# Performance work log

Measured on AMD Instinct MI355X. Metric: run time of the kernel, lower is better.

Reference implementation:

```python
import jax, jax.numpy as jnp
import numpy as np

NU, NI = 100000, 100000   # num users / items
DU, DI = 128, 128         # input feature dims
H, O = 256, 256           # hidden_channels, out_channels
ER, EA = 500000, 500000   # edges: reviews, also_bought


def setup_inputs() -> dict:
    key = jax.random.key(0)
    ks = jax.random.split(key, 30)

    def W(k, i, o):
        return jax.random.normal(k, (i, o), jnp.float32) * np.float32(1.0 / np.sqrt(i))

    return {
        "x_user": jax.random.normal(ks[0], (NU, DU), jnp.float32),
        "x_item": jax.random.normal(ks[1], (NI, DI), jnp.float32),
        "src_rev": jax.random.randint(ks[2], (ER,), 0, NU, jnp.int32),
        "dst_rev": jax.random.randint(ks[3], (ER,), 0, NI, jnp.int32),
        "src_ab": jax.random.randint(ks[4], (EA,), 0, NI, jnp.int32),
        "dst_ab": jax.random.randint(ks[5], (EA,), 0, NI, jnp.int32),
        # layer 1 (SAGEConv per edge type): lin_l (neighbor), lin_r (root), bias on lin_l
        "Wl1_rev": W(ks[6], DU, H), "Wr1_rev": W(ks[7], DI, H), "b1_rev": jnp.zeros((H,), jnp.float32),
        "Wl1_rrev": W(ks[8], DI, H), "Wr1_rrev": W(ks[9], DU, H), "b1_rrev": jnp.zeros((H,), jnp.float32),
        "Wl1_ab": W(ks[10], DI, H), "Wr1_ab": W(ks[11], DI, H), "b1_ab": jnp.zeros((H,), jnp.float32),
        # layer 2
        "Wl2_rev": W(ks[12], H, O), "Wr2_rev": W(ks[13], H, O), "b2_rev": jnp.zeros((O,), jnp.float32),
        "Wl2_rrev": W(ks[14], H, O), "Wr2_rrev": W(ks[15], H, O), "b2_rrev": jnp.zeros((O,), jnp.float32),
        "Wl2_ab": W(ks[16], H, O), "Wr2_ab": W(ks[17], H, O), "b2_ab": jnp.zeros((O,), jnp.float32),
    }


def sage_conv(x_src, x_dst, src, dst, Wl, b, Wr):
    """PyG SAGEConv: lin_l(mean of neighbor feats) + lin_r(x_dst); mean of empty set = 0."""
    n_dst = x_dst.shape[0]
    msg_sum = jax.ops.segment_sum(x_src[src], dst, num_segments=n_dst)   # [n_dst, d_src]
    cnt = jax.ops.segment_sum(jnp.ones(dst.shape, x_src.dtype), dst, num_segments=n_dst)
    mean = msg_sum / jnp.maximum(cnt, 1.0)[:, None]
    return mean @ Wl + b + x_dst @ Wr


def reference(x_user, x_item, src_rev, dst_rev, src_ab, dst_ab,
              Wl1_rev, Wr1_rev, b1_rev, Wl1_rrev, Wr1_rrev, b1_rrev, Wl1_ab, Wr1_ab, b1_ab,
              Wl2_rev, Wr2_rev, b2_rev, Wl2_rrev, Wr2_rrev, b2_rrev, Wl2_ab, Wr2_ab, b2_ab):
    # layer 1 + HeteroConv sum aggregation across edge types per dst node type
    h_item = (sage_conv(x_user, x_item, src_rev, dst_rev, Wl1_rev, b1_rev, Wr1_rev)
              + sage_conv(x_item, x_item, src_ab, dst_ab, Wl1_ab, b1_ab, Wr1_ab))
    # rev_reviews = transpose of reviews: item -> user
    h_user = sage_conv(x_item, x_user, dst_rev, src_rev, Wl1_rrev, b1_rrev, Wr1_rrev)
    h_item = jax.nn.relu(h_item)
    h_user = jax.nn.relu(h_user)
    # layer 2
    o_item = (sage_conv(h_user, h_item, src_rev, dst_rev, Wl2_rev, b2_rev, Wr2_rev)
              + sage_conv(h_item, h_item, src_ab, dst_ab, Wl2_ab, b2_ab, Wr2_ab))
    o_user = sage_conv(h_item, h_user, dst_rev, src_rev, Wl2_rrev, b2_rrev, Wr2_rrev)
    return (o_user, o_item)
```

## Files before the change

kernel.cpp:

```cpp
#include <hip/hip_runtime.h>
#include <hip/hip_bf16.h>

#define NN    100000
#define MPAD  100096
#define ER_   500000
#define EA_   500000
#define NCH   25
#define F_RELU 2

typedef __attribute__((ext_vector_type(8))) _Float16 f16x8;
typedef __attribute__((ext_vector_type(4))) float f32x4;
typedef __attribute__((address_space(3))) uint lds_uint;
typedef const __attribute__((address_space(1))) uint g_uint;

union H8 { uint4 u; _Float16 h[8]; };
union H1 { _Float16 h; ushort u; };

__device__ __forceinline__ ushort f2h(float f) { H1 c; c.h = (_Float16)f; return c.u; }

__global__ void count3(const int* __restrict__ dst_rev, const int* __restrict__ dst_ab,
                       const int* __restrict__ src_rev, int* __restrict__ cnt ) {
    int i = blockIdx.x * blockDim.x + threadIdx.x;
    if (i < ER_)                 atomicAdd(&cnt[dst_rev[i]], 1);
    else if (i < ER_ + EA_)      atomicAdd(&cnt[NN + dst_ab[i - ER_]], 1);
    else if (i < ER_ + EA_ + ER_) atomicAdd(&cnt[2 * NN + src_rev[i - ER_ - EA_]], 1);
}

__global__ void fill3(const int* __restrict__ dst_rev, const int* __restrict__ src_rev,
                      const int* __restrict__ dst_ab, const int* __restrict__ src_ab,
                      const int* __restrict__ pA, const int* __restrict__ pB,
                      const int* __restrict__ pC, int* __restrict__ cur ,
                      int* __restrict__ colA, int* __restrict__ colB, int* __restrict__ colC) {
    int i = blockIdx.x * blockDim.x + threadIdx.x;
    if (i < ER_) {
        int d = dst_rev[i];
        colA[pA[d] + atomicAdd(&cur[d], 1)] = src_rev[i];
    } else if (i < ER_ + EA_) {
        int e = i - ER_, d = dst_ab[e];
        colB[pB[d] + atomicAdd(&cur[NN + d], 1)] = src_ab[e];
    } else if (i < ER_ + EA_ + ER_) {
        int e = i - ER_ - EA_, d = src_rev[e];
        colC[pC[d] + atomicAdd(&cur[2 * NN + d], 1)] = dst_rev[e];
    }
}

__global__ void scan_part(const int* __restrict__ cnt , int* __restrict__ part) {
    int b = blockIdx.x, a = b / NCH, c = b % NCH;
    const int* src = cnt + a * NN;
    int base = c * 4096 + threadIdx.x * 16;
    int s = 0;
    #pragma unroll
    for (int k = 0; k < 16; k += 4) {
        int i = base + k;
        if (i + 3 < NN) { int4 v = *(const int4*)(src + i); s += v.x + v.y + v.z + v.w; }
        else { for (int j = 0; j < 4; j++) if (i + j < NN) s += src[i + j]; }
    }
    __shared__ int ws[4];
    int lane = threadIdx.x & 63, wid = threadIdx.x >> 6;
    #pragma unroll
    for (int o = 32; o > 0; o >>= 1) s += __shfl_down(s, o, 64);
    if (lane == 0) ws[wid] = s;
    __syncthreads();
    if (threadIdx.x == 0) part[b] = ws[0] + ws[1] + ws[2] + ws[3];
}

__global__ void scan_off(const int* __restrict__ part, int* __restrict__ choff,
                         int* __restrict__ pA, int* __restrict__ pB, int* __restrict__ pC) {
    int a = threadIdx.x;
    if (a < 3) {
        int acc = 0;
        for (int c = 0; c < NCH; c++) { choff[a * NCH + c] = acc; acc += part[a * NCH + c]; }
        int* p = (a == 0) ? pA : (a == 1) ? pB : pC;
        p[NN] = acc;
    }
}

__global__ void scan_apply(const int* __restrict__ cnt, const int* __restrict__ choff,
                           int* __restrict__ pA, int* __restrict__ pB, int* __restrict__ pC) {
    int b = blockIdx.x, a = b / NCH, c = b % NCH;
    const int* src = cnt + a * NN;
    int* ptr = (a == 0) ? pA : (a == 1) ? pB : pC;
    int tid = threadIdx.x, lane = tid & 63, wid = tid >> 6;
    int base = c * 4096 + tid * 16;
    int v[16], s = 0;
    #pragma unroll
    for (int k = 0; k < 16; k++) { int i = base + k; v[k] = (i < NN) ? src[i] : 0; s += v[k]; }
    int isc = s;
    #pragma unroll
    for (int o = 1; o < 64; o <<= 1) { int t = __shfl_up(isc, o, 64); if (lane >= o) isc += t; }
    __shared__ int wsum[4];
    if (lane == 63) wsum[wid] = isc;
    __syncthreads();
    int woff = 0;
    for (int wj = 0; wj < wid; wj++) woff += wsum[wj];
    int excl = choff[a * NCH + c] + woff + (isc - s);
    #pragma unroll
    for (int k = 0; k < 16; k++) { int i = base + k; if (i < NN) ptr[i] = excl; excl += v[k]; }
}

struct PrepArgs {
    const float* xsrc[2]; ushort* xdst[2];
    const float* W0[10]; const float* W1[10]; ushort* T[10];
};

__global__ void prep_all(PrepArgs A) {
    const long CVB = (long)MPAD * 128 / 8 / 256;
    long b = blockIdx.x;
    if (b < 2 * CVB) {
        int which = (b >= CVB);
        long lb = b - which * CVB;
        long i = (lb * 256 + threadIdx.x) * 8;
        const float* x = A.xsrc[which];
        ushort* o = A.xdst[which];
        float4 v0 = {0.f,0.f,0.f,0.f}, v1 = {0.f,0.f,0.f,0.f};
        if (i < (long)NN * 128) { v0 = *(const float4*)(x + i); v1 = *(const float4*)(x + i + 4); }
        H8 r;
        r.h[0]=(_Float16)v0.x; r.h[1]=(_Float16)v0.y; r.h[2]=(_Float16)v0.z; r.h[3]=(_Float16)v0.w;
        r.h[4]=(_Float16)v1.x; r.h[5]=(_Float16)v1.y; r.h[6]=(_Float16)v1.z; r.h[7]=(_Float16)v1.w;
        *(uint4*)(o + i) = r.u;
        return;
    }
    long j = (b - 2 * CVB) * 256 + threadIdx.x;
    int idx, rem, K;
    if (j < 5 * 32768) { idx = j >> 15; rem = j & 32767; K = 128; }
    else {
        long j2 = j - 5 * 32768;
        if (j2 >= 5L * 65536) return;
        idx = 5 + (int)(j2 >> 16); rem = (int)(j2 & 65535); K = 256;
    }
    int k = rem >> 8, n = rem & 255;
    float v = A.W0[idx][rem];
    if (A.W1[idx]) v += A.W1[idx][rem];
    A.T[idx][n * K + k] = f2h(v);
}

__global__ void agg3_128(const ushort* __restrict__ xu, const ushort* __restrict__ xi,
                         const int* __restrict__ pA, const int* __restrict__ cA,
                         const int* __restrict__ pB, const int* __restrict__ cB,
                         const int* __restrict__ pC, const int* __restrict__ cC,
                         ushort* __restrict__ sA, ushort* __restrict__ sB,
                         ushort* __restrict__ sC) {
    const int SEG = MPAD * 16 / 256;
    int seg = blockIdx.x / SEG, lb = blockIdx.x % SEG;
    const ushort* x; const int* ptr; const int* col; ushort* out;
    if (seg == 0)      { x = xu; ptr = pA; col = cA; out = sA; }
    else if (seg == 1) { x = xi; ptr = pB; col = cB; out = sB; }
    else               { x = xi; ptr = pC; col = cC; out = sC; }
    int g = lb * 256 + threadIdx.x;
    int node = g >> 4, l = g & 15;
    if (node >= MPAD) return;
    size_t ob = (size_t)node * 128 + l * 8;
    if (node >= NN) { *(uint4*)(out + ob) = make_uint4(0,0,0,0); return; }
    int p0 = ptr[node], p1 = ptr[node + 1];
    float a[8] = {0.f,0.f,0.f,0.f,0.f,0.f,0.f,0.f};
    for (int e = p0; e < p1; ++e) {
        H8 v; v.u = *(const uint4*)(x + (size_t)col[e] * 128 + l * 8);
        #pragma unroll
        for (int k = 0; k < 8; k++) a[k] += (float)v.h[k];
    }
    float inv = (p1 > p0) ? 1.0f / (float)(p1 - p0) : 0.0f;
    H8 r;
    #pragma unroll
    for (int k = 0; k < 8; k++) r.h[k] = (_Float16)(a[k] * inv);
    *(uint4*)(out + ob) = r.u;
}

__global__ void agg3_256(const ushort* __restrict__ hU, const ushort* __restrict__ hI,
                         const int* __restrict__ pA, const int* __restrict__ cA,
                         const int* __restrict__ pB, const int* __restrict__ cB,
                         const int* __restrict__ pC, const int* __restrict__ cC,
                         ushort* __restrict__ sA, ushort* __restrict__ sB,
                         ushort* __restrict__ sC) {
    const int SEG = MPAD * 32 / 256;
    int seg = blockIdx.x / SEG, lb = blockIdx.x % SEG;
    const ushort* x; const int* ptr; const int* col; ushort* out;
    if (seg == 0)      { x = hU; ptr = pA; col = cA; out = sA; }
    else if (seg == 1) { x = hI; ptr = pB; col = cB; out = sB; }
    else               { x = hI; ptr = pC; col = cC; out = sC; }
    int g = lb * 256 + threadIdx.x;
    int node = g >> 5, l = g & 31;
    if (node >= MPAD) return;
    size_t ob = (size_t)node * 256 + l * 8;
    if (node >= NN) { *(uint4*)(out + ob) = make_uint4(0,0,0,0); return; }
    int p0 = ptr[node], p1 = ptr[node + 1];
    float a[8] = {0.f,0.f,0.f,0.f,0.f,0.f,0.f,0.f};
    for (int e = p0; e < p1; ++e) {
        H8 v; v.u = *(const uint4*)(x + (size_t)col[e] * 256 + l * 8);
        #pragma unroll
        for (int k = 0; k < 8; k++) a[k] += (float)v.h[k];
    }
    float inv = (p1 > p0) ? 1.0f / (float)(p1 - p0) : 0.0f;
    H8 r;
    #pragma unroll
    for (int k = 0; k < 8; k++) r.h[k] = (_Float16)(a[k] * inv);
    *(uint4*)(out + ob) = r.u;
}

struct GP {
    const ushort *A0, *W0, *A1, *W1, *A2, *W2;
    int ksh0, ksh1, ksh2;
    int c1, c2, S;
};

__global__ __launch_bounds__(256)
void gemm2x(GP Pa, const float* b0a, const float* b1a, float* Cfa, ushort* Cha, int fla,
            GP Pb, const float* b0b, const float* b1b, float* Cfb, ushort* Chb, int flb) {
    GP P; const float *b0, *b1; float* Cf; ushort* Ch; int flags;
    if (blockIdx.z == 0) { P = Pa; b0 = b0a; b1 = b1a; Cf = Cfa; Ch = Cha; flags = fla; }
    else                 { P = Pb; b0 = b0b; b1 = b1b; Cf = Cfb; Ch = Chb; flags = flb; }

    __shared__ ushort sA[128 * 64];
    __shared__ ushort sW[128 * 64];
    const int tid = threadIdx.x;
    const int m0 = blockIdx.x * 128, n0 = blockIdx.y * 128;
    const int lane = tid & 63, w = tid >> 6;
    const int wr = (w >> 1) * 64, wc = (w & 1) * 64;
    const int fcol = lane & 15, fq = lane >> 4;
    const int srow = tid >> 3, sc = tid & 7;

    f32x4 acc[4][4];
    #pragma unroll
    for (int i = 0; i < 4; i++)
        #pragma unroll
        for (int j = 0; j < 4; j++) acc[i][j] = (f32x4){0.f,0.f,0.f,0.f};

    #pragma unroll 1
    for (int t = 0; t < P.S; ++t) {
        int p = (t >= P.c1) + (t >= P.c2);
        const ushort* A = (p == 2) ? P.A2 : (p == 1) ? P.A1 : P.A0;
        const ushort* W = (p == 2) ? P.W2 : (p == 1) ? P.W1 : P.W0;
        int ksh  = (p == 2) ? P.ksh2 : (p == 1) ? P.ksh1 : P.ksh0;
        int base = (p == 2) ? P.c2 : (p == 1) ? P.c1 : 0;
        int k0 = (t - base) << 6;

        #pragma unroll
        for (int ii = 0; ii < 4; ++ii) {
            int row = ii * 32 + srow;
            int q = sc ^ (row & 7);
            const ushort* srcA = A + (((size_t)(m0 + row)) << ksh) + k0 + q * 8;
            const ushort* srcW = W + (((size_t)(n0 + row)) << ksh) + k0 + q * 8;
            __builtin_amdgcn_global_load_lds((g_uint*)srcA,
                (lds_uint*)(sA + row * 64 + sc * 8), 16, 0, 0);
            __builtin_amdgcn_global_load_lds((g_uint*)srcW,
                (lds_uint*)(sW + row * 64 + sc * 8), 16, 0, 0);
        }
        __syncthreads();

        #pragma unroll
        for (int kk = 0; kk < 2; ++kk) {
            f16x8 a[4], b[4];
            #pragma unroll
            for (int i = 0; i < 4; ++i) {
                int ra = wr + i * 16 + fcol;
                int s = (fq + kk * 4) ^ (ra & 7);
                a[i] = *(const f16x8*)(sA + ra * 64 + s * 8);
            }
            #pragma unroll
            for (int j = 0; j < 4; ++j) {
                int rw = wc + j * 16 + fcol;
                int s = (fq + kk * 4) ^ (rw & 7);
                b[j] = *(const f16x8*)(sW + rw * 64 + s * 8);
            }
            #pragma unroll
            for (int i = 0; i < 4; ++i)
                #pragma unroll
                for (int j = 0; j < 4; ++j)
                    acc[i][j] = __builtin_amdgcn_mfma_f32_16x16x32_f16(a[i], b[j], acc[i][j], 0, 0, 0);
        }
        __syncthreads();
    }

    const bool relu = flags & F_RELU;
    float bb[4];
    #pragma unroll
    for (int j = 0; j < 4; ++j) {
        int cg = n0 + wc + j * 16 + fcol;
        float v = 0.f;
        if (b0) v += b0[cg];
        if (b1) v += b1[cg];
        bb[j] = v;
    }
    #pragma unroll
    for (int i = 0; i < 4; ++i) {
        #pragma unroll
        for (int r = 0; r < 4; ++r) {
            int gm = m0 + wr + i * 16 + fq * 4 + r;
            if (gm >= NN) continue;
            size_t rowb = (size_t)gm * 256;
            #pragma unroll
            for (int j = 0; j < 4; ++j) {
                size_t idx = rowb + n0 + wc + j * 16 + fcol;
                float v = acc[i][j][r] + bb[j];
                if (relu) v = fmaxf(v, 0.f);
                if (Ch) Ch[idx] = f2h(v);
                else    Cf[idx] = v;
            }
        }
    }
}

extern "C" void kernel_launch(void* const* d_in, const int* in_sizes, int n_in,
                              void* d_out, int out_size, void* d_ws, size_t ws_size,
                              hipStream_t stream) {
    const float* x_user = (const float*)d_in[0];
    const float* x_item = (const float*)d_in[1];
    const int* src_rev  = (const int*)d_in[2];
    const int* dst_rev  = (const int*)d_in[3];
    const int* src_ab   = (const int*)d_in[4];
    const int* dst_ab   = (const int*)d_in[5];
    const float* Wl1_rev  = (const float*)d_in[6];
    const float* Wr1_rev  = (const float*)d_in[7];
    const float* b1_rev   = (const float*)d_in[8];
    const float* Wl1_rrev = (const float*)d_in[9];
    const float* Wr1_rrev = (const float*)d_in[10];
    const float* b1_rrev  = (const float*)d_in[11];
    const float* Wl1_ab   = (const float*)d_in[12];
    const float* Wr1_ab   = (const float*)d_in[13];
    const float* b1_ab    = (const float*)d_in[14];
    const float* Wl2_rev  = (const float*)d_in[15];
    const float* Wr2_rev  = (const float*)d_in[16];
    const float* b2_rev   = (const float*)d_in[17];
    const float* Wl2_rrev = (const float*)d_in[18];
    const float* Wr2_rrev = (const float*)d_in[19];
    const float* b2_rrev  = (const float*)d_in[20];
    const float* Wl2_ab   = (const float*)d_in[21];
    const float* Wr2_ab   = (const float*)d_in[22];
    const float* b2_ab    = (const float*)d_in[23];

    float* o_user = (float*)d_out;
    float* o_item = (float*)d_out + (size_t)NN * 256;

    char* ws = (char*)d_ws;
    size_t off = 0;
    auto alloc = [&](size_t bytes) -> void* {
        void* p = ws + off;
        off += (bytes + 255) & ~(size_t)255;
        return p;
    };
    const size_t P256 = (size_t)MPAD * 256 * 2;
    const size_t P128 = (size_t)MPAD * 128 * 2;
    ushort* xu     = (ushort*)alloc(P128);
    ushort* xi     = (ushort*)alloc(P128);
    ushort* slabA  = (ushort*)alloc(P128);
    ushort* slabB  = (ushort*)alloc(P128);
    ushort* slabC  = (ushort*)alloc(P128);
    ushort* hI     = (ushort*)alloc(P256);
    ushort* hU     = (ushort*)alloc(P256);
    ushort* s2A    = (ushort*)alloc(P256);
    ushort* s2B    = (ushort*)alloc(P256);
    ushort* s2C    = (ushort*)alloc(P256);
    const size_t W1SZ = 128 * 256 * 2, W2SZ = 256 * 256 * 2;
    ushort* wt_l1rev  = (ushort*)alloc(W1SZ);
    ushort* wt_l1ab   = (ushort*)alloc(W1SZ);
    ushort* wt_l1rrev = (ushort*)alloc(W1SZ);
    ushort* wt_r1c    = (ushort*)alloc(W1SZ);
    ushort* wt_r1rrev = (ushort*)alloc(W1SZ);
    ushort* wt_l2rev  = (ushort*)alloc(W2SZ);
    ushort* wt_l2ab   = (ushort*)alloc(W2SZ);
    ushort* wt_l2rrev = (ushort*)alloc(W2SZ);
    ushort* wt_r2c    = (ushort*)alloc(W2SZ);
    ushort* wt_r2rrev = (ushort*)alloc(W2SZ);
    int* ptrA = (int*)alloc((NN + 1) * 4);
    int* ptrB = (int*)alloc((NN + 1) * 4);
    int* ptrC = (int*)alloc((NN + 1) * 4);
    int* colA = (int*)alloc((size_t)ER_ * 4);
    int* colB = (int*)alloc((size_t)EA_ * 4);
    int* colC = (int*)alloc((size_t)ER_ * 4);
    int* cnt3 = (int*)alloc((size_t)3 * NN * 4);
    int* part  = (int*)alloc(3 * NCH * 4);
    int* choff = (int*)alloc(3 * NCH * 4);

    const int TPB = 256;
    const int NE3 = ER_ + EA_ + ER_;
    dim3 e3grid((NE3 + TPB - 1) / TPB);

    hipMemsetAsync(cnt3, 0, (size_t)3 * NN * 4, stream);
    count3<<<e3grid, TPB, 0, stream>>>(dst_rev, dst_ab, src_rev, cnt3);
    scan_part<<<3 * NCH, TPB, 0, stream>>>(cnt3, part);
    scan_off<<<1, 64, 0, stream>>>(part, choff, ptrA, ptrB, ptrC);
    scan_apply<<<3 * NCH, TPB, 0, stream>>>(cnt3, choff, ptrA, ptrB, ptrC);
    hipMemsetAsync(cnt3, 0, (size_t)3 * NN * 4, stream);
    fill3<<<e3grid, TPB, 0, stream>>>(dst_rev, src_rev, dst_ab, src_ab,
                                      ptrA, ptrB, ptrC, cnt3, colA, colB, colC);

    PrepArgs PA;
    PA.xsrc[0] = x_user; PA.xdst[0] = xu;
    PA.xsrc[1] = x_item; PA.xdst[1] = xi;
    const float* W0s[10] = {Wl1_rev, Wl1_ab, Wl1_rrev, Wr1_rev, Wr1_rrev,
                            Wl2_rev, Wl2_ab, Wl2_rrev, Wr2_rev, Wr2_rrev};
    const float* W1s[10] = {nullptr, nullptr, nullptr, Wr1_ab, nullptr,
                            nullptr, nullptr, nullptr, Wr2_ab, nullptr};
    ushort* Ts[10] = {wt_l1rev, wt_l1ab, wt_l1rrev, wt_r1c, wt_r1rrev,
                      wt_l2rev, wt_l2ab, wt_l2rrev, wt_r2c, wt_r2rrev};
    for (int i = 0; i < 10; i++) { PA.W0[i] = W0s[i]; PA.W1[i] = W1s[i]; PA.T[i] = Ts[i]; }
    const long CVB = (long)MPAD * 128 / 8 / 256;
    const long WPB = (5 * 32768 + 5 * 65536 + 255) / 256;
    prep_all<<<(int)(2 * CVB + WPB), TPB, 0, stream>>>(PA);

    dim3 ggrid(MPAD / 128, 2, 2);

    auto mkGP = [&](const ushort* a0, const ushort* w0, int K0,
                    const ushort* a1, const ushort* w1, int K1,
                    const ushort* a2, const ushort* w2, int K2) {
        GP P;
        P.A0 = a0; P.W0 = w0;
        P.A1 = a1 ? a1 : a0; P.W1 = w1 ? w1 : w0;
        P.A2 = a2 ? a2 : a0; P.W2 = w2 ? w2 : w0;
        P.ksh0 = (K0 == 256) ? 8 : 7;
        P.ksh1 = (K1 == 256) ? 8 : 7;
        P.ksh2 = (K2 == 256) ? 8 : 7;
        P.c1 = K0 >> 6; P.c2 = P.c1 + (K1 >> 6); P.S = P.c2 + (K2 >> 6);
        return P;
    };

    agg3_128<<<3 * (MPAD * 16 / 256), TPB, 0, stream>>>(xu, xi, ptrA, colA, ptrB, colB,
                                                        ptrC, colC, slabA, slabB, slabC);
    {
        GP P0 = mkGP(slabA, wt_l1rev, 128, slabB, wt_l1ab, 128, xi, wt_r1c, 128);
        GP P1 = mkGP(slabC, wt_l1rrev, 128, xu, wt_r1rrev, 128, nullptr, nullptr, 0);
        gemm2x<<<ggrid, TPB, 0, stream>>>(P0, b1_rev, b1_ab, nullptr, hI, F_RELU,
                                          P1, b1_rrev, nullptr, nullptr, hU, F_RELU);
    }

    agg3_256<<<3 * (MPAD * 32 / 256), TPB, 0, stream>>>(hU, hI, ptrA, colA, ptrB, colB,
                                                        ptrC, colC, s2A, s2B, s2C);
    {
        GP P0 = mkGP(s2A, wt_l2rev, 256, s2B, wt_l2ab, 256, hI, wt_r2c, 256);
        GP P1 = mkGP(s2C, wt_l2rrev, 256, hU, wt_r2rrev, 256, nullptr, nullptr, 0);
        gemm2x<<<ggrid, TPB, 0, stream>>>(P0, b2_rev, b2_ab, o_item, nullptr, 0,
                                          P1, b2_rrev, nullptr, o_user, nullptr, 0);
    }
}
```

Baseline: 856.5 us.

## Double-buffer GEMM LDS tiles and split/unroll neighbor aggregation by feature half

The GEMM now uses two LDS buffers so the next K-tile's global-to-LDS loads are issued before computing on the current tile, which removes one barrier per iteration and overlaps load latency with MFMA work. The aggregation kernels are split into two feature halves handled by separate block ranges, so each node uses half as many threads per pass. Their edge loop is also unrolled by four, putting several independent gathers in flight at once. The cost is doubled LDS per GEMM block, which may lower occupancy, and the aggregation kernels now read the CSR index arrays twice.

```diff
diff --git a/kernel.cpp b/kernel.cpp
--- a/kernel.cpp
+++ b/kernel.cpp
@@ -140,21 +140,41 @@
                          const int* __restrict__ pC, const int* __restrict__ cC,
                          ushort* __restrict__ sA, ushort* __restrict__ sB,
                          ushort* __restrict__ sC) {
-    const int SEG = MPAD * 16 / 256;
+    const int SEG = MPAD * 8 / 256;
     int seg = blockIdx.x / SEG, lb = blockIdx.x % SEG;
+    int dir = seg % 3, half = seg / 3;
     const ushort* x; const int* ptr; const int* col; ushort* out;
-    if (seg == 0)      { x = xu; ptr = pA; col = cA; out = sA; }
-    else if (seg == 1) { x = xi; ptr = pB; col = cB; out = sB; }
+    if (dir == 0)      { x = xu; ptr = pA; col = cA; out = sA; }
+    else if (dir == 1) { x = xi; ptr = pB; col = cB; out = sB; }
     else               { x = xi; ptr = pC; col = cC; out = sC; }
     int g = lb * 256 + threadIdx.x;
-    int node = g >> 4, l = g & 15;
+    int node = g >> 3, l = g & 7;
     if (node >= MPAD) return;
-    size_t ob = (size_t)node * 128 + l * 8;
+    int doff = half * 64 + l * 8;
+    size_t ob = (size_t)node * 128 + doff;
     if (node >= NN) { *(uint4*)(out + ob) = make_uint4(0,0,0,0); return; }
+    const ushort* xb = x + doff;
     int p0 = ptr[node], p1 = ptr[node + 1];
     float a[8] = {0.f,0.f,0.f,0.f,0.f,0.f,0.f,0.f};
-    for (int e = p0; e < p1; ++e) {
-        H8 v; v.u = *(const uint4*)(x + (size_t)col[e] * 128 + l * 8);
+    int e = p0;
+    for (; e + 4 <= p1; e += 4) {
+        int c0 = col[e], c1 = col[e+1], c2 = col[e+2], c3 = col[e+3];
+        H8 v0, v1, v2, v3;
+        v0.u = *(const uint4*)(xb + (size_t)c0 * 128);
+        v1.u = *(const uint4*)(xb + (size_t)c1 * 128);
+        v2.u = *(const uint4*)(xb + (size_t)c2 * 128);
+        v3.u = *(const uint4*)(xb + (size_t)c3 * 128);
+        #pragma unroll
+        for (int k = 0; k < 8; k++) a[k] += (float)v0.h[k];
+        #pragma unroll
+        for (int k = 0; k < 8; k++) a[k] += (float)v1.h[k];
+        #pragma unroll
+        for (int k = 0; k < 8; k++) a[k] += (float)v2.h[k];
+        #pragma unroll
+        for (int k = 0; k < 8; k++) a[k] += (float)v3.h[k];
+    }
+    for (; e < p1; ++e) {
+        H8 v; v.u = *(const uint4*)(xb + (size_t)col[e] * 128);
         #pragma unroll
         for (int k = 0; k < 8; k++) a[k] += (float)v.h[k];
     }
@@ -171,21 +191,41 @@
                          const int* __restrict__ pC, const int* __restrict__ cC,
                          ushort* __restrict__ sA, ushort* __restrict__ sB,
                          ushort* __restrict__ sC) {
-    const int SEG = MPAD * 32 / 256;
+    const int SEG = MPAD * 16 / 256;
     int seg = blockIdx.x / SEG, lb = blockIdx.x % SEG;
+    int dir = seg % 3, half = seg / 3;
     const ushort* x; const int* ptr; const int* col; ushort* out;
-    if (seg == 0)      { x = hU; ptr = pA; col = cA; out = sA; }
-    else if (seg == 1) { x = hI; ptr = pB; col = cB; out = sB; }
+    if (dir == 0)      { x = hU; ptr = pA; col = cA; out = sA; }
+    else if (dir == 1) { x = hI; ptr = pB; col = cB; out = sB; }
     else               { x = hI; ptr = pC; col = cC; out = sC; }
     int g = lb * 256 + threadIdx.x;
-    int node = g >> 5, l = g & 31;
+    int node = g >> 4, l = g & 15;
     if (node >= MPAD) return;
-    size_t ob = (size_t)node * 256 + l * 8;
+    int doff = half * 128 + l * 8;
+    size_t ob = (size_t)node * 256 + doff;
     if (node >= NN) { *(uint4*)(out + ob) = make_uint4(0,0,0,0); return; }
+    const ushort* xb = x + doff;
     int p0 = ptr[node], p1 = ptr[node + 1];
     float a[8] = {0.f,0.f,0.f,0.f,0.f,0.f,0.f,0.f};
-    for (int e = p0; e < p1; ++e) {
-        H8 v; v.u = *(const uint4*)(x + (size_t)col[e] * 256 + l * 8);
+    int e = p0;
+    for (; e + 4 <= p1; e += 4) {
+        int c0 = col[e], c1 = col[e+1], c2 = col[e+2], c3 = col[e+3];
+        H8 v0, v1, v2, v3;
+        v0.u = *(const uint4*)(xb + (size_t)c0 * 256);
+        v1.u = *(const uint4*)(xb + (size_t)c1 * 256);
+        v2.u = *(const uint4*)(xb + (size_t)c2 * 256);
+        v3.u = *(const uint4*)(xb + (size_t)c3 * 256);
+        #pragma unroll
+        for (int k = 0; k < 8; k++) a[k] += (float)v0.h[k];
+        #pragma unroll
+        for (int k = 0; k < 8; k++) a[k] += (float)v1.h[k];
+        #pragma unroll
+        for (int k = 0; k < 8; k++) a[k] += (float)v2.h[k];
+        #pragma unroll
+        for (int k = 0; k < 8; k++) a[k] += (float)v3.h[k];
+    }
+    for (; e < p1; ++e) {
+        H8 v; v.u = *(const uint4*)(xb + (size_t)col[e] * 256);
         #pragma unroll
         for (int k = 0; k < 8; k++) a[k] += (float)v.h[k];
     }
@@ -209,8 +249,8 @@
     if (blockIdx.z == 0) { P = Pa; b0 = b0a; b1 = b1a; Cf = Cfa; Ch = Cha; flags = fla; }
     else                 { P = Pb; b0 = b0b; b1 = b1b; Cf = Cfb; Ch = Chb; flags = flb; }
 
-    __shared__ ushort sA[128 * 64];
-    __shared__ ushort sW[128 * 64];
+    __shared__ ushort sA[2][128 * 64];
+    __shared__ ushort sW[2][128 * 64];
     const int tid = threadIdx.x;
     const int m0 = blockIdx.x * 128, n0 = blockIdx.y * 128;
     const int lane = tid & 63, w = tid >> 6;
@@ -224,15 +264,14 @@
         #pragma unroll
         for (int j = 0; j < 4; j++) acc[i][j] = (f32x4){0.f,0.f,0.f,0.f};
 
-    #pragma unroll 1
-    for (int t = 0; t < P.S; ++t) {
+    auto stage = [&](int t, int buf) {
+        if (t >= P.S) return;
         int p = (t >= P.c1) + (t >= P.c2);
         const ushort* A = (p == 2) ? P.A2 : (p == 1) ? P.A1 : P.A0;
         const ushort* W = (p == 2) ? P.W2 : (p == 1) ? P.W1 : P.W0;
         int ksh  = (p == 2) ? P.ksh2 : (p == 1) ? P.ksh1 : P.ksh0;
         int base = (p == 2) ? P.c2 : (p == 1) ? P.c1 : 0;
         int k0 = (t - base) << 6;
-
         #pragma unroll
         for (int ii = 0; ii < 4; ++ii) {
             int row = ii * 32 + srow;
@@ -240,12 +279,20 @@
             const ushort* srcA = A + (((size_t)(m0 + row)) << ksh) + k0 + q * 8;
             const ushort* srcW = W + (((size_t)(n0 + row)) << ksh) + k0 + q * 8;
             __builtin_amdgcn_global_load_lds((g_uint*)srcA,
-                (lds_uint*)(sA + row * 64 + sc * 8), 16, 0, 0);
+                (lds_uint*)(&sA[buf][row * 64 + sc * 8]), 16, 0, 0);
             __builtin_amdgcn_global_load_lds((g_uint*)srcW,
-                (lds_uint*)(sW + row * 64 + sc * 8), 16, 0, 0);
+                (lds_uint*)(&sW[buf][row * 64 + sc * 8]), 16, 0, 0);
         }
+    };
+
+    stage(0, 0);
+    int cur = 0;
+    #pragma unroll 1
+    for (int t = 0; t < P.S; ++t) {
         __syncthreads();
-
+        stage(t + 1, cur ^ 1);
+        const ushort* bA = sA[cur];
+        const ushort* bW = sW[cur];
         #pragma unroll
         for (int kk = 0; kk < 2; ++kk) {
             f16x8 a[4], b[4];
@@ -253,13 +300,13 @@
             for (int i = 0; i < 4; ++i) {
                 int ra = wr + i * 16 + fcol;
                 int s = (fq + kk * 4) ^ (ra & 7);
-                a[i] = *(const f16x8*)(sA + ra * 64 + s * 8);
+                a[i] = *(const f16x8*)(bA + ra * 64 + s * 8);
             }
             #pragma unroll
             for (int j = 0; j < 4; ++j) {
                 int rw = wc + j * 16 + fcol;
                 int s = (fq + kk * 4) ^ (rw & 7);
-                b[j] = *(const f16x8*)(sW + rw * 64 + s * 8);
+                b[j] = *(const f16x8*)(bW + rw * 64 + s * 8);
             }
             #pragma unroll
             for (int i = 0; i < 4; ++i)
@@ -267,7 +314,7 @@
                 for (int j = 0; j < 4; ++j)
                     acc[i][j] = __builtin_amdgcn_mfma_f32_16x16x32_f16(a[i], b[j], acc[i][j], 0, 0, 0);
         }
-        __syncthreads();
+        cur ^= 1;
     }
 
     const bool relu = flags & F_RELU;
@@ -413,8 +460,8 @@
         return P;
     };
 
-    agg3_128<<<3 * (MPAD * 16 / 256), TPB, 0, stream>>>(xu, xi, ptrA, colA, ptrB, colB,
-                                                        ptrC, colC, slabA, slabB, slabC);
+    agg3_128<<<6 * (MPAD * 8 / 256), TPB, 0, stream>>>(xu, xi, ptrA, colA, ptrB, colB,
+                                                       ptrC, colC, slabA, slabB, slabC);
     {
         GP P0 = mkGP(slabA, wt_l1rev, 128, slabB, wt_l1ab, 128, xi, wt_r1c, 128);
         GP P1 = mkGP(slabC, wt_l1rrev, 128, xu, wt_r1rrev, 128, nullptr, nullptr, 0);
@@ -422,7 +469,7 @@
                                           P1, b1_rrev, nullptr, nullptr, hU, F_RELU);
     }
 
-    agg3_256<<<3 * (MPAD * 32 / 256), TPB, 0, stream>>>(hU, hI, ptrA, colA, ptrB, colB,
+    agg3_256<<<6 * (MPAD * 16 / 256), TPB, 0, stream>>>(hU, hI, ptrA, colA, ptrB, colB,
                                                         ptrC, colC, s2A, s2B, s2C);
     {
         GP P0 = mkGP(s2A, wt_l2rev, 256, s2B, wt_l2ab, 256, hI, wt_r2c, 256);
```

Result: slower. 911.5 us (+6.4%).
